# Performance work log

Measured on AMD Instinct MI355X. Metric: run time of the kernel, lower is better.

Reference implementation:

```python
import jax, jax.numpy as jnp
import numpy as np
import math

B, S, E = 4, 2048, 1024
H, D = 16, 64

def setup_inputs() -> dict:
    key = jax.random.key(0)
    ks = jax.random.split(key, 9)
    sE = 1.0 / math.sqrt(E)
    sHD = 1.0 / math.sqrt(H * D)
    return {
        "x": jax.random.normal(ks[0], (B, S, E), jnp.float32),
        "Wq": jax.random.normal(ks[1], (H, E, D), jnp.float32) * sE,
        "bq": jax.random.normal(ks[2], (H, D), jnp.float32) * sE,
        "Wk": jax.random.normal(ks[3], (H, E, D), jnp.float32) * sE,
        "bk": jax.random.normal(ks[4], (H, D), jnp.float32) * sE,
        "Wv": jax.random.normal(ks[5], (H, E, D), jnp.float32) * sE,
        "bv": jax.random.normal(ks[6], (H, D), jnp.float32) * sE,
        "Wo": jax.random.normal(ks[7], (E, E), jnp.float32) * sHD,
        "bo": jax.random.normal(ks[8], (E,), jnp.float32) * sHD,
    }

def reference(x, Wq, bq, Wk, bk, Wv, bv, Wo, bo):
    # Projections for all heads at once: [B,H,S,D]
    Q = jnp.einsum('bse,hed->bhsd', x, Wq) + bq[:, None, :]
    K = jnp.einsum('bse,hed->bhsd', x, Wk) + bk[:, None, :]
    V = jnp.einsum('bse,hed->bhsd', x, Wv) + bv[:, None, :]
    scale = 1.0 / math.sqrt(D)
    scores = jnp.einsum('bhsd,bhtd->bhst', Q, K) * scale  # [B,H,S,S]
    S_len = x.shape[1]
    causal = jnp.tril(jnp.ones((S_len, S_len), dtype=bool))
    scores = jnp.where(causal, scores, -jnp.inf)
    probs = jax.nn.softmax(scores, axis=-1)
    ctx = jnp.einsum('bhst,bhtd->bhsd', probs, V)  # [B,H,S,D]
    # concat heads: head order matches torch cat over ModuleList
    conc = jnp.transpose(ctx, (0, 2, 1, 3)).reshape(x.shape[0], S_len, H * D)
    # torch Linear: y = conc @ W.T + b ; Wo stored as [out,in]=[E,E]
    out = conc @ Wo.T + bo
    # dropout is identity in eval mode
    return out
```

## Files before the change

kernel.cpp:

```cpp
#include <hip/hip_runtime.h>
#include <math.h>

constexpr int Bn = 4;
constexpr int Sn = 2048;
constexpr int En = 1024;
constexpr int Hn = 16;
constexpr int Dn = 64;

typedef float f32x4 __attribute__((ext_vector_type(4)));
typedef short s16x8 __attribute__((ext_vector_type(8)));
typedef short s16x4 __attribute__((ext_vector_type(4)));

__device__ __forceinline__ short f2bf(float f) {
    unsigned u = __builtin_bit_cast(unsigned, f);
    unsigned r = (u + 0x7fffu + ((u >> 16) & 1u)) >> 16;
    return (short)r;
}

__device__ __forceinline__ void glds16(const short* g, short* l) {
    __builtin_amdgcn_global_load_lds(
        (const __attribute__((address_space(1))) short*)g,
        (__attribute__((address_space(3))) short*)l, 16, 0, 0);
}

__global__ __launch_bounds__(256) void conv_x_kernel(
    const float* __restrict__ x, short* __restrict__ y)
{
    size_t i = ((size_t)blockIdx.x * 256 + threadIdx.x) * 4;
    float4 v = *(const float4*)(x + i);
    s16x4 o;
    o[0] = f2bf(v.x); o[1] = f2bf(v.y); o[2] = f2bf(v.z); o[3] = f2bf(v.w);
    *(s16x4*)(y + i) = o;
}

__global__ __launch_bounds__(256) void build_wcat_kernel(
    const float* __restrict__ Wq, const float* __restrict__ bq,
    const float* __restrict__ Wk, const float* __restrict__ bk,
    const float* __restrict__ Wv, const float* __restrict__ bv,
    short* __restrict__ Wcat, float* __restrict__ bias_cat)
{
    const int et = blockIdx.x, h = blockIdx.y, p = blockIdx.z;
    const float* W  = (p == 0) ? Wq : (p == 1) ? Wk : Wv;
    const float* bb = (p == 0) ? bq : (p == 1) ? bk : bv;
    const float* Wh = W + (size_t)h * En * Dn;

    __shared__ float T[64][65];
    const int tid = threadIdx.x;
    #pragma unroll
    for (int it = 0; it < 16; it++) {
        int idx = tid + it * 256;
        int e = idx >> 6, d = idx & 63;
        T[d][e] = Wh[(size_t)(et * 64 + e) * Dn + d];
    }
    __syncthreads();
    #pragma unroll
    for (int it = 0; it < 16; it++) {
        int idx = tid + it * 256;
        int d = idx >> 6, e = idx & 63;
        Wcat[(size_t)(p * 1024 + h * 64 + d) * En + et * 64 + e] = f2bf(T[d][e]);
    }
    if (et == 0 && tid < 64)
        bias_cat[p * 1024 + h * 64 + tid] = bb[h * 64 + tid];
}

__global__ __launch_bounds__(256) void conv_wo_kernel(
    const float* __restrict__ Wo, short* __restrict__ Wob)
{
    const size_t base = (size_t)blockIdx.x * En;
    #pragma unroll
    for (int i = 0; i < 4; i++) {
        int k = threadIdx.x + i * 256;
        Wob[base + k] = f2bf(Wo[base + k]);
    }
}

__global__ __launch_bounds__(256) void gemm_bt_kernel(
    const short* __restrict__ A,
    const short* __restrict__ Bt,
    const float* __restrict__ bias,
    float* __restrict__ outF,
    short* __restrict__ Qb, short* __restrict__ Kb, short* __restrict__ Vtb,
    int mode)
{
    constexpr int K = En;
    const int m0 = blockIdx.x * 128;
    const int n0 = blockIdx.y * 128;

    __shared__ short As[128 * 64];
    __shared__ short Bs[128 * 64];

    const int tid  = threadIdx.x;
    const int w    = tid >> 6;
    const int lane = tid & 63;
    const int quad = lane >> 4;
    const int l15  = lane & 15;
    const int wr = (w >> 1) * 64;
    const int wc = (w & 1) * 64;

    f32x4 acc[4][4];
    #pragma unroll
    for (int i = 0; i < 4; i++)
        #pragma unroll
        for (int j = 0; j < 4; j++)
            #pragma unroll
            for (int e = 0; e < 4; e++) acc[i][j][e] = 0.f;

    for (int k0 = 0; k0 < K; k0 += 64) {
        #pragma unroll
        for (int r = 0; r < 4; r++) {
            int c   = (r * 4 + w) * 64 + lane;
            int row = c >> 3;
            int lp  = (c & 7) ^ (row & 7);
            glds16(A + (size_t)(m0 + row) * K + k0 + lp * 8,
                   As + (r * 4 + w) * 512);
            glds16(Bt + (size_t)(n0 + row) * K + k0 + lp * 8,
                   Bs + (r * 4 + w) * 512);
        }
        __syncthreads();

        #pragma unroll
        for (int ks = 0; ks < 2; ks++) {
            s16x8 af[4], bfr[4];
            #pragma unroll
            for (int mt = 0; mt < 4; mt++) {
                int row = wr + mt * 16 + l15;
                af[mt] = *(const s16x8*)&As[row * 64 + (((ks * 4 + quad) ^ (l15 & 7)) * 8)];
            }
            #pragma unroll
            for (int nt = 0; nt < 4; nt++) {
                int row = wc + nt * 16 + l15;
                bfr[nt] = *(const s16x8*)&Bs[row * 64 + (((ks * 4 + quad) ^ (l15 & 7)) * 8)];
            }
            #pragma unroll
            for (int mt = 0; mt < 4; mt++)
                #pragma unroll
                for (int nt = 0; nt < 4; nt++)
                    acc[mt][nt] = __builtin_amdgcn_mfma_f32_16x16x32_bf16(
                        af[mt], bfr[nt], acc[mt][nt], 0, 0, 0);
        }
        __syncthreads();
    }

    if (mode == 0) {
        #pragma unroll
        for (int mt = 0; mt < 4; mt++) {
            #pragma unroll
            for (int reg = 0; reg < 4; reg++) {
                int m = m0 + wr + mt * 16 + quad * 4 + reg;
                #pragma unroll
                for (int nt = 0; nt < 4; nt++) {
                    int n = n0 + wc + nt * 16 + l15;
                    outF[(size_t)m * En + n] = acc[mt][nt][reg] + bias[n];
                }
            }
        }
    } else {
        const int p = (n0 + wc) >> 10;
        const float qs = (p == 0) ? 0.125f : 1.0f;
        #pragma unroll
        for (int mt = 0; mt < 4; mt++) {
            #pragma unroll
            for (int reg = 0; reg < 4; reg++) {
                int m = m0 + wr + mt * 16 + quad * 4 + reg;
                int b = m >> 11, s = m & 2047;
                #pragma unroll
                for (int nt = 0; nt < 4; nt++) {
                    int n = n0 + wc + nt * 16 + l15;
                    int h = (n >> 6) & 15, d = n & 63;
                    short v = f2bf((acc[mt][nt][reg] + bias[n]) * qs);
                    if (p == 0)
                        Qb[(((size_t)(b * Hn + h)) * Sn + s) * Dn + d] = v;
                    else if (p == 1)
                        Kb[(((size_t)(b * Hn + h)) * Sn + s) * Dn + d] = v;
                    else
                        Vtb[(((size_t)(b * Hn + h)) * Dn + d) * Sn + s] = v;
                }
            }
        }
    }
}

__global__ __launch_bounds__(256) void attn_mfma_kernel(
    const short* __restrict__ Q, const short* __restrict__ K,
    const short* __restrict__ Vt, short* __restrict__ Cb)
{
    constexpr int PP = 72;
    const int i  = blockIdx.x;
    const int bh = blockIdx.y;
    const int b = bh >> 4, h = bh & 15;
    const int t0 = i, t1 = 31 - i;

    __shared__ short Ks[64 * 64];
    __shared__ short Vts[64 * 64];
    __shared__ short Ps[128 * PP];
    __shared__ float l_sh[128];

    const int tid  = threadIdx.x;
    const int w    = tid >> 6;
    const int lane = tid & 63;
    const int quad = lane >> 4;
    const int l15  = lane & 15;

    const short* Kp = K + (size_t)bh * Sn * Dn;
    const short* Vp = Vt + (size_t)bh * Dn * Sn;

    const int tf[2] = {t0, t1};
    s16x8 aq[2][2];
    #pragma unroll
    for (int f = 0; f < 2; f++)
        #pragma unroll
        for (int ks = 0; ks < 2; ks++)
            aq[f][ks] = *(const s16x8*)(
                Q + ((size_t)bh * Sn + tf[f] * 64 + w * 16 + l15) * Dn +
                ks * 32 + quad * 8);

    f32x4 acc[2][4];
    #pragma unroll
    for (int f = 0; f < 2; f++)
        #pragma unroll
        for (int nt = 0; nt < 4; nt++)
            #pragma unroll
            for (int e = 0; e < 4; e++) acc[f][nt][e] = 0.f;
    float lpart[2] = {0.f, 0.f};

    for (int kt = 0; kt <= t1; kt++) {
        #pragma unroll
        for (int r = 0; r < 2; r++) {
            int c   = (r * 4 + w) * 64 + lane;
            int row = c >> 3;
            int lp  = (c & 7) ^ (row & 7);
            glds16(Kp + (size_t)(kt * 64 + row) * Dn + lp * 8,
                   Ks + (r * 4 + w) * 512);
            glds16(Vp + (size_t)row * Sn + kt * 64 + lp * 8,
                   Vts + (r * 4 + w) * 512);
        }
        __syncthreads();

        #pragma unroll
        for (int f = 0; f < 2; f++) {
            if (kt > tf[f]) continue;
            f32x4 st[4];
            #pragma unroll
            for (int nt = 0; nt < 4; nt++)
                #pragma unroll
                for (int e = 0; e < 4; e++) st[nt][e] = 0.f;
            #pragma unroll
            for (int ks = 0; ks < 2; ks++) {
                #pragma unroll
                for (int nt = 0; nt < 4; nt++) {
                    s16x8 bk = *(const s16x8*)&Ks[(nt * 16 + l15) * 64 +
                                                  (((ks * 4 + quad) ^ (l15 & 7)) * 8)];
                    st[nt] = __builtin_amdgcn_mfma_f32_16x16x32_bf16(
                        bk, aq[f][ks], st[nt], 0, 0, 0);
                }
            }
            const bool diag = (kt == tf[f]);
            #pragma unroll
            for (int nt = 0; nt < 4; nt++) {
                unsigned tb[4];
                #pragma unroll
                for (int reg = 0; reg < 4; reg++) {
                    float v = __expf(st[nt][reg]);
                    if (diag && (nt * 16 + quad * 4 + reg) > (w * 16 + l15))
                        v = 0.f;
                    unsigned tv = __builtin_bit_cast(unsigned, v) & 0xFFFF0000u;
                    tb[reg] = tv;
                    lpart[f] += __builtin_bit_cast(float, tv);
                }
                uint2 pk;
                pk.x = (tb[0] >> 16) | tb[1];
                pk.y = (tb[2] >> 16) | tb[3];
                *(uint2*)&Ps[(f * 64 + w * 16 + l15) * PP + nt * 16 + quad * 4] = pk;
            }
        }

        #pragma unroll
        for (int ks = 0; ks < 2; ks++) {
            s16x8 bv[4];
            #pragma unroll
            for (int nt = 0; nt < 4; nt++)
                bv[nt] = *(const s16x8*)&Vts[(nt * 16 + l15) * 64 +
                                             (((ks * 4 + quad) ^ (l15 & 7)) * 8)];
            #pragma unroll
            for (int f = 0; f < 2; f++) {
                if (kt > tf[f]) continue;
                s16x8 ap = *(const s16x8*)&Ps[(f * 64 + w * 16 + l15) * PP +
                                              ks * 32 + quad * 8];
                #pragma unroll
                for (int nt = 0; nt < 4; nt++)
                    acc[f][nt] = __builtin_amdgcn_mfma_f32_16x16x32_bf16(
                        ap, bv[nt], acc[f][nt], 0, 0, 0);
            }
        }
        __syncthreads();
    }

    #pragma unroll
    for (int f = 0; f < 2; f++) {
        float l = lpart[f];
        l += __shfl_xor(l, 16);
        l += __shfl_xor(l, 32);
        if (quad == 0) l_sh[f * 64 + w * 16 + l15] = l;
    }
    __syncthreads();

    #pragma unroll
    for (int f = 0; f < 2; f++) {
        #pragma unroll
        for (int reg = 0; reg < 4; reg++) {
            int s = tf[f] * 64 + w * 16 + quad * 4 + reg;
            float inv = 1.f / l_sh[f * 64 + w * 16 + quad * 4 + reg];
            #pragma unroll
            for (int nt = 0; nt < 4; nt++) {
                int d = nt * 16 + l15;
                Cb[((size_t)(b * Sn + s)) * En + h * Dn + d] =
                    f2bf(acc[f][nt][reg] * inv);
            }
        }
    }
}

extern "C" void kernel_launch(void* const* d_in, const int* in_sizes, int n_in,
                              void* d_out, int out_size, void* d_ws, size_t ws_size,
                              hipStream_t stream) {
    const float* x  = (const float*)d_in[0];
    const float* Wq = (const float*)d_in[1];
    const float* bq = (const float*)d_in[2];
    const float* Wk = (const float*)d_in[3];
    const float* bk = (const float*)d_in[4];
    const float* Wv = (const float*)d_in[5];
    const float* bv = (const float*)d_in[6];
    const float* Wo = (const float*)d_in[7];
    const float* bo = (const float*)d_in[8];
    float* out = (float*)d_out;

    const size_t XS   = (size_t)Bn * Sn * En;
    const size_t WCS  = (size_t)3 * En * Hn * Dn;
    const size_t WOS  = (size_t)En * En;
    const size_t QSZ  = (size_t)Bn * Hn * Sn * Dn;

    short* Ax    = (short*)d_ws;
    short* Wcat  = Ax + XS;
    short* Wob   = Wcat + WCS;
    float* biasc = (float*)(Wob + WOS);
    short* Qb    = (short*)(biasc + 3072);
    short* Kb    = Qb + QSZ;
    short* Vtb   = Kb + QSZ;
    short* Cbf   = Vtb + QSZ;

    conv_x_kernel<<<dim3(XS / (256 * 4)), 256, 0, stream>>>(x, Ax);
    build_wcat_kernel<<<dim3(16, 16, 3), 256, 0, stream>>>(Wq, bq, Wk, bk, Wv, bv,
                                                           Wcat, biasc);
    conv_wo_kernel<<<dim3(En), 256, 0, stream>>>(Wo, Wob);

    gemm_bt_kernel<<<dim3((Bn * Sn) / 128, 3072 / 128), 256, 0, stream>>>(
        Ax, Wcat, biasc, nullptr, Qb, Kb, Vtb, 1);

    attn_mfma_kernel<<<dim3(16, Bn * Hn), 256, 0, stream>>>(Qb, Kb, Vtb, Cbf);

    gemm_bt_kernel<<<dim3((Bn * Sn) / 128, En / 128), 256, 0, stream>>>(
        Cbf, Wob, bo, out, nullptr, nullptr, nullptr, 0);
}
```

Before: 283.8 us.

## Enlarge GEMM tiles to 256x128 with 512 threads and vectorize V-transpose stores

The projection GEMM now uses 256x128 output tiles computed by eight waves instead of 128x128 tiles by four waves. Each B tile is reused across twice as many rows, which cuts global and LDS traffic per FLOP. In the QKV epilogue, the transposed V store now packs four consecutive sequence positions into one 8-byte write instead of four scattered 2-byte writes. The trade-off is half as many blocks: the output projection gets only 256 blocks, and LDS use per block is larger, which may hurt occupancy.

```diff
diff --git a/kernel.cpp b/kernel.cpp
--- a/kernel.cpp
+++ b/kernel.cpp
@@ -74,7 +74,7 @@
     }
 }
 
-__global__ __launch_bounds__(256) void gemm_bt_kernel(
+__global__ __launch_bounds__(512) void gemm_bt_kernel(
     const short* __restrict__ A,
     const short* __restrict__ Bt,
     const float* __restrict__ bias,
@@ -83,10 +83,10 @@
     int mode)
 {
     constexpr int K = En;
-    const int m0 = blockIdx.x * 128;
+    const int m0 = blockIdx.x * 256;
     const int n0 = blockIdx.y * 128;
 
-    __shared__ short As[128 * 64];
+    __shared__ short As[256 * 64];
     __shared__ short Bs[128 * 64];
 
     const int tid  = threadIdx.x;
@@ -108,13 +108,19 @@
     for (int k0 = 0; k0 < K; k0 += 64) {
         #pragma unroll
         for (int r = 0; r < 4; r++) {
-            int c   = (r * 4 + w) * 64 + lane;
+            int c   = (r * 8 + w) * 64 + lane;
             int row = c >> 3;
             int lp  = (c & 7) ^ (row & 7);
             glds16(A + (size_t)(m0 + row) * K + k0 + lp * 8,
-                   As + (r * 4 + w) * 512);
+                   As + (r * 8 + w) * 512);
+        }
+        #pragma unroll
+        for (int r = 0; r < 2; r++) {
+            int c   = (r * 8 + w) * 64 + lane;
+            int row = c >> 3;
+            int lp  = (c & 7) ^ (row & 7);
             glds16(Bt + (size_t)(n0 + row) * K + k0 + lp * 8,
-                   Bs + (r * 4 + w) * 512);
+                   Bs + (r * 8 + w) * 512);
         }
         __syncthreads();
 
@@ -156,24 +162,38 @@
         }
     } else {
         const int p = (n0 + wc) >> 10;
-        const float qs = (p == 0) ? 0.125f : 1.0f;
-        #pragma unroll
-        for (int mt = 0; mt < 4; mt++) {
-            #pragma unroll
-            for (int reg = 0; reg < 4; reg++) {
-                int m = m0 + wr + mt * 16 + quad * 4 + reg;
+        if (p < 2) {
+            const float qs = (p == 0) ? 0.125f : 1.0f;
+            short* dst = (p == 0) ? Qb : Kb;
+            #pragma unroll
+            for (int mt = 0; mt < 4; mt++) {
+                #pragma unroll
+                for (int reg = 0; reg < 4; reg++) {
+                    int m = m0 + wr + mt * 16 + quad * 4 + reg;
+                    int b = m >> 11, s = m & 2047;
+                    #pragma unroll
+                    for (int nt = 0; nt < 4; nt++) {
+                        int n = n0 + wc + nt * 16 + l15;
+                        int h = (n >> 6) & 15, d = n & 63;
+                        dst[(((size_t)(b * Hn + h)) * Sn + s) * Dn + d] =
+                            f2bf((acc[mt][nt][reg] + bias[n]) * qs);
+                    }
+                }
+            }
+        } else {
+            #pragma unroll
+            for (int mt = 0; mt < 4; mt++) {
+                int m = m0 + wr + mt * 16 + quad * 4;
                 int b = m >> 11, s = m & 2047;
                 #pragma unroll
                 for (int nt = 0; nt < 4; nt++) {
                     int n = n0 + wc + nt * 16 + l15;
                     int h = (n >> 6) & 15, d = n & 63;
-                    short v = f2bf((acc[mt][nt][reg] + bias[n]) * qs);
-                    if (p == 0)
-                        Qb[(((size_t)(b * Hn + h)) * Sn + s) * Dn + d] = v;
-                    else if (p == 1)
-                        Kb[(((size_t)(b * Hn + h)) * Sn + s) * Dn + d] = v;
-                    else
-                        Vtb[(((size_t)(b * Hn + h)) * Dn + d) * Sn + s] = v;
+                    s16x4 pk;
+                    #pragma unroll
+                    for (int reg = 0; reg < 4; reg++)
+                        pk[reg] = f2bf(acc[mt][nt][reg] + bias[n]);
+                    *(s16x4*)(Vtb + (((size_t)(b * Hn + h)) * Dn + d) * Sn + s) = pk;
                 }
             }
         }
@@ -353,11 +373,11 @@
                                                            Wcat, biasc);
     conv_wo_kernel<<<dim3(En), 256, 0, stream>>>(Wo, Wob);
 
-    gemm_bt_kernel<<<dim3((Bn * Sn) / 128, 3072 / 128), 256, 0, stream>>>(
+    gemm_bt_kernel<<<dim3((Bn * Sn) / 256, 3072 / 128), 512, 0, stream>>>(
         Ax, Wcat, biasc, nullptr, Qb, Kb, Vtb, 1);
 
     attn_mfma_kernel<<<dim3(16, Bn * Hn), 256, 0, stream>>>(Qb, Kb, Vtb, Cbf);
 
-    gemm_bt_kernel<<<dim3((Bn * Sn) / 128, En / 128), 256, 0, stream>>>(
+    gemm_bt_kernel<<<dim3((Bn * Sn) / 256, En / 128), 512, 0, stream>>>(
         Cbf, Wob, bo, out, nullptr, nullptr, nullptr, 0);
 }
```

After: 260.4 us. 8.2% less time.
